# Optimization experiments

Hardware: AMD Instinct MI355X
Metric: run time of the kernel (lower is better)

The kernel has to match this reference:

```python
import jax, jax.numpy as jnp
import numpy as np

B, T, E, NH = 2, 1024, 512, 8


def setup_inputs() -> dict:
    key = jax.random.key(0)
    ks = jax.random.split(key, 7)
    s = 0.02
    return {
        "x": jax.random.normal(ks[0], (B, T, E), dtype=jnp.float32),
        "W_qkv": jax.random.normal(ks[1], (E, 3 * E), dtype=jnp.float32) * s,
        "b_qkv": jax.random.normal(ks[2], (3 * E,), dtype=jnp.float32) * s,
        "W_od": jax.random.normal(ks[3], (E, 2 * NH), dtype=jnp.float32) * s,
        "b_od": jax.random.normal(ks[4], (2 * NH,), dtype=jnp.float32) * s,
        "W_out": jax.random.normal(ks[5], (E, E), dtype=jnp.float32) * s,
        "b_out": jax.random.normal(ks[6], (E,), dtype=jnp.float32) * s,
        "length": T,
    }


def reference(x, W_qkv, b_qkv, W_od, b_od, W_out, b_out, length):
    b, t, e = x.shape
    nh = W_od.shape[1] // 2
    hd = e // nh
    scaling = float(hd) ** (-0.5)

    qkv = x @ W_qkv + b_qkv
    Q, K, V = jnp.split(qkv, 3, axis=-1)  # each (b, t, e)

    od = Q @ W_od + b_od  # (b, t, 2*nh)
    offset, duration = jnp.split(od, 2, axis=-1)
    offset = jnp.tanh(offset) * length
    duration = jax.nn.sigmoid(duration) * length

    qidx = jnp.arange(length, dtype=x.dtype)[None, :, None]  # (1, t, 1)
    anchor = qidx + offset  # (b, t, nh)

    # 'b t nh -> (b nh) t'
    anchor = anchor.transpose(0, 2, 1).reshape(b * nh, t)
    duration = duration.transpose(0, 2, 1).reshape(b * nh, t)

    start = anchor - duration
    end = anchor + duration
    bl = jnp.floor(start)          # left bound index
    br = jnp.ceil(end)             # right bound index
    al = jnp.floor(anchor)         # anchor left index
    ar = al + 1                    # anchor right index
    dist_al = anchor - al          # anchor_dist_l

    r = jnp.arange(length, dtype=x.dtype)[None, None, :]  # (1, 1, t)

    def pmask(idx):  # point mask (bnh, t, t), float
        return (r == idx[:, :, None]).astype(x.dtype)

    point_weight = (1.0
                    + (bl - start)[:, :, None] * pmask(bl)
                    + (end - br)[:, :, None] * pmask(br)
                    + dist_al[:, :, None] * pmask(ar)
                    + (1.0 - dist_al)[:, :, None] * pmask(al))

    attn_mask = (r < bl[:, :, None]) | (r > br[:, :, None])  # (bnh, t, t) bool

    def heads(z):  # 'b t (nh hd) -> (b nh) t hd'
        return z.reshape(b, t, nh, hd).transpose(0, 2, 1, 3).reshape(b * nh, t, hd)

    Qh, Kh, Vh = heads(Q), heads(K), heads(V)

    scores = jnp.einsum('bic,brc->bir', Qh, Kh) * scaling
    scores = scores * point_weight
    scores = jnp.where(attn_mask, jnp.asarray(-1e8, x.dtype), scores)
    attn = jax.nn.softmax(scores, axis=-1)

    out = jnp.einsum('bir,brc->bic', attn, Vh)  # (bnh, t, hd)
    out = out.reshape(b, nh, t, hd).transpose(0, 2, 1, 3).reshape(b, t, e)
    return out @ W_out + b_out
```

## Files before the change

kernel.cpp:

```cpp
#include <hip/hip_runtime.h>

typedef unsigned short ushort_t;
typedef short s16x8 __attribute__((ext_vector_type(8)));
typedef float f32x4 __attribute__((ext_vector_type(4)));

#define DEVINL __device__ __forceinline__

DEVINL ushort_t f2b(float f) {
  union { float f; unsigned int u; } v; v.f = f;
  unsigned int r = (v.u + 0x7fffu + ((v.u >> 16) & 1u)) >> 16;
  return (ushort_t)r;
}

DEVINL ushort_t f2b_hw(float f) {
  union { __bf16 h; ushort_t u; } cv;
  cv.h = (__bf16)f;
  return cv.u;
}

__global__ __launch_bounds__(256) void prep_kernel(
    const float* __restrict__ Wqkv, const float* __restrict__ bq,
    const float* __restrict__ Wod, const float* __restrict__ bod,
    const float* __restrict__ Wout,
    ushort_t* __restrict__ WqkvT, ushort_t* __restrict__ WoT,
    float* __restrict__ Wcomb, float* __restrict__ bcomb)
{
  __shared__ ushort_t tile[64 * 72];
  const int b = blockIdx.x;
  const int tid = threadIdx.x;

  if (b < 256) {
    const float* in;
    ushort_t* out;
    int N, bx, by;
    if (b < 192) { in = Wqkv; out = WqkvT; N = 1536; bx = b % 24; by = b / 24; }
    else         { in = Wout; out = WoT;   N = 512;  bx = (b - 192) % 8; by = (b - 192) / 8; }
    const int K = 512;
    const int n0 = bx * 64, k0 = by * 64;
    const int cr = tid >> 4;
    const int cc = (tid & 15) * 4;
#pragma unroll
    for (int p = 0; p < 4; p++) {
      int k = k0 + p * 16 + cr;
      float4 v = *(const float4*)(in + k * N + n0 + cc);
      ushort4 o; o.x = f2b(v.x); o.y = f2b(v.y); o.z = f2b(v.z); o.w = f2b(v.w);
      *(ushort4*)(tile + (p * 16 + cr) * 72 + cc) = o;
    }
    __syncthreads();
#pragma unroll
    for (int p = 0; p < 4; p++) {
      int n = n0 + p * 16 + cr;
      ushort4 v;
      v.x = tile[(cc + 0) * 72 + p * 16 + cr];
      v.y = tile[(cc + 1) * 72 + p * 16 + cr];
      v.z = tile[(cc + 2) * 72 + p * 16 + cr];
      v.w = tile[(cc + 3) * 72 + p * 16 + cr];
      *(ushort4*)(out + n * K + k0 + cc) = v;
    }
    return;
  }

  const int w = tid >> 6, lane = tid & 63;
  const int c = (b - 256) * 4 + w;
  if (c > 512) return;
  float a[8];
  const float* src = (c < 512) ? (Wqkv + c * 1536 + lane * 8) : (bq + lane * 8);
  float4 a0 = *(const float4*)(src);
  float4 a1 = *(const float4*)(src + 4);
  a[0]=a0.x; a[1]=a0.y; a[2]=a0.z; a[3]=a0.w;
  a[4]=a1.x; a[5]=a1.y; a[6]=a1.z; a[7]=a1.w;

  float s[16];
#pragma unroll
  for (int j = 0; j < 16; j++) s[j] = 0.f;
#pragma unroll
  for (int i = 0; i < 8; i++) {
    const float* wp = Wod + (lane * 8 + i) * 16;
#pragma unroll
    for (int j = 0; j < 16; j++) s[j] += a[i] * wp[j];
  }
#pragma unroll
  for (int mask = 1; mask < 64; mask <<= 1)
#pragma unroll
    for (int j = 0; j < 16; j++) s[j] += __shfl_xor(s[j], mask);

  if (lane < 16) {
    if (c < 512) Wcomb[c * 16 + lane] = s[lane];
    else         bcomb[lane] = s[lane] + bod[lane];
  }
}

__global__ __launch_bounds__(256) void od_kernel(
    const float* __restrict__ x, const float* __restrict__ Wcomb,
    const float* __restrict__ bcomb, const int* __restrict__ lenp,
    float* __restrict__ params, ushort_t* __restrict__ xb)
{
  const int w = threadIdx.x >> 6, lane = threadIdx.x & 63;
  const int m = blockIdx.x * 4 + w;
  int li = lenp[0];
  float len = (li > 0 && li < 1048576) ? (float)li : 1024.0f;

  const float* qp = x + m * 512 + lane * 8;
  float q[8];
  float4 qa = *(const float4*)(qp);
  float4 qb = *(const float4*)(qp + 4);
  q[0]=qa.x; q[1]=qa.y; q[2]=qa.z; q[3]=qa.w;
  q[4]=qb.x; q[5]=qb.y; q[6]=qb.z; q[7]=qb.w;

  s16x8 ov;
#pragma unroll
  for (int i = 0; i < 8; i++) ov[i] = (short)f2b(q[i]);
  *(s16x8*)(xb + m * 512 + lane * 8) = ov;

  float s[16];
#pragma unroll
  for (int j = 0; j < 16; j++) s[j] = 0.f;
#pragma unroll
  for (int i = 0; i < 8; i++) {
    const float* wp = Wcomb + (lane * 8 + i) * 16;
#pragma unroll
    for (int j = 0; j < 16; j++) s[j] += q[i] * wp[j];
  }
#pragma unroll
  for (int mask = 1; mask < 64; mask <<= 1)
#pragma unroll
    for (int j = 0; j < 16; j++) s[j] += __shfl_xor(s[j], mask);

  if (lane < 8) {
    int h = lane;
    int bb = m >> 10, t = m & 1023;
    float odo = s[h] + bcomb[h];
    float odd = s[8 + h] + bcomb[8 + h];
    float offset = tanhf(odo) * len;
    float dur = len / (1.f + expf(-odd));
    float anchor = (float)t + offset;
    float start = anchor - dur, end = anchor + dur;
    float bl = floorf(start), br = ceilf(end);
    float al = floorf(anchor);
    float da = anchor - al;
    float* pp = params + ((bb * 8 + h) * 1024 + t) * 6;
    pp[0] = bl; pp[1] = br; pp[2] = al;
    pp[3] = bl - start; pp[4] = end - br; pp[5] = da;
  }
}

__global__ __launch_bounds__(256) void qkv_gemm_kernel(
    const ushort_t* __restrict__ xb, const ushort_t* __restrict__ WT,
    const float* __restrict__ bqkv,
    ushort_t* __restrict__ Qh, ushort_t* __restrict__ Kh, ushort_t* __restrict__ VT)
{
  __shared__ ushort_t As[64 * 32];
  __shared__ ushort_t Bs[128 * 32];
  const int tid = threadIdx.x;
  const int lane = tid & 63, w = tid >> 6;
  const int wr = w >> 1, wc = w & 1;
  const int quad = lane >> 4, l16 = lane & 15;
  const int m0 = blockIdx.y * 64, n0 = blockIdx.x * 128;

  f32x4 acc[2][4];
#pragma unroll
  for (int i = 0; i < 2; i++)
#pragma unroll
    for (int j = 0; j < 4; j++) acc[i][j] = f32x4{0.f, 0.f, 0.f, 0.f};

  const int idx = tid * 8;
  const int ra = idx >> 5, ca = idx & 31;
  const int rb1 = (idx + 2048) >> 5, cb1 = (idx + 2048) & 31;

  for (int k0 = 0; k0 < 512; k0 += 32) {
    s16x8 va  = *(const s16x8*)(xb + (m0 + ra) * 512 + k0 + ca);
    s16x8 vb0 = *(const s16x8*)(WT + (n0 + ra) * 512 + k0 + ca);
    s16x8 vb1 = *(const s16x8*)(WT + (n0 + rb1) * 512 + k0 + cb1);
    __syncthreads();
    *(s16x8*)(As + idx) = va;
    *(s16x8*)(Bs + idx) = vb0;
    *(s16x8*)(Bs + idx + 2048) = vb1;
    __syncthreads();

    s16x8 af[2], bfr[4];
#pragma unroll
    for (int mt = 0; mt < 2; mt++)
      af[mt] = *(const s16x8*)(As + (wr * 32 + mt * 16 + l16) * 32 + quad * 8);
#pragma unroll
    for (int nt = 0; nt < 4; nt++)
      bfr[nt] = *(const s16x8*)(Bs + (wc * 64 + nt * 16 + l16) * 32 + quad * 8);
#pragma unroll
    for (int mt = 0; mt < 2; mt++)
#pragma unroll
      for (int nt = 0; nt < 4; nt++)
        acc[mt][nt] = __builtin_amdgcn_mfma_f32_16x16x32_bf16(af[mt], bfr[nt], acc[mt][nt], 0, 0, 0);
  }

#pragma unroll
  for (int nt = 0; nt < 4; nt++) {
    int c = n0 + wc * 64 + nt * 16 + l16;
    float bias = bqkv[c];
    int which = c >> 9;
    int e = c & 511;
    int h = e >> 6, d = e & 63;
#pragma unroll
    for (int mt = 0; mt < 2; mt++) {
      int mbase = m0 + wr * 32 + mt * 16 + quad * 4;
      int bb = mbase >> 10, t = mbase & 1023;
      int bh = bb * 8 + h;
      if (which == 2) {
        ushort4 pk;
        pk.x = f2b(acc[mt][nt][0] + bias);
        pk.y = f2b(acc[mt][nt][1] + bias);
        pk.z = f2b(acc[mt][nt][2] + bias);
        pk.w = f2b(acc[mt][nt][3] + bias);
        *(ushort4*)(VT + (bh * 64 + d) * 1024 + t) = pk;
      } else {
        ushort_t* dst = (which == 0) ? Qh : Kh;
        float sc = (which == 0) ? 0.125f : 1.0f;
#pragma unroll
        for (int rr = 0; rr < 4; rr++)
          dst[(bh * 1024 + t + rr) * 64 + d] = f2b((acc[mt][nt][rr] + bias) * sc);
      }
    }
  }
}

__global__ __launch_bounds__(256, 3) void attn_kernel(
    const ushort_t* __restrict__ Qh, const ushort_t* __restrict__ Kh,
    const ushort_t* __restrict__ VT, const float* __restrict__ params,
    ushort_t* __restrict__ Oh)
{
  __shared__ ushort_t Plds[4 * 16 * 72];
  __shared__ float Om[4][16][65];
  __shared__ float lwS[4][16];

  const int tid = threadIdx.x;
  const int lane = tid & 63, w = tid >> 6;
  const int quad = lane >> 4, l16 = lane & 15;
  const int bh = blockIdx.x;
  const int mrow = blockIdx.y * 16;
  ushort_t* Pw = Plds + w * (16 * 72);

  s16x8 aq0 = *(const s16x8*)(Qh + (bh * 1024 + mrow + l16) * 64 + quad * 8);
  s16x8 aq1 = *(const s16x8*)(Qh + (bh * 1024 + mrow + l16) * 64 + 32 + quad * 8);

  float bl[4], br[4], al[4], wl[4], wr2[4], da[4];
  float lo = 1.0e9f, hi = -1.0e9f;
#pragma unroll
  for (int rr = 0; rr < 4; rr++) {
    int row = mrow + quad * 4 + rr;
    const float* pp = params + (bh * 1024 + row) * 6;
    bl[rr] = pp[0]; br[rr] = pp[1]; al[rr] = pp[2];
    wl[rr] = pp[3]; wr2[rr] = pp[4]; da[rr] = pp[5];
    bool empty = (br[rr] < 0.f) || (bl[rr] > 1023.f);
    float lo_r = empty ? 0.f    : fmaxf(bl[rr], 0.f);
    float hi_r = empty ? 1023.f : fminf(br[rr], 1023.f);
    lo = fminf(lo, lo_r); hi = fmaxf(hi, hi_r);
  }
  lo = fminf(lo, __shfl_xor(lo, 16));
  lo = fminf(lo, __shfl_xor(lo, 32));
  hi = fmaxf(hi, __shfl_xor(hi, 16));
  hi = fmaxf(hi, __shfl_xor(hi, 32));
  const int tlo = ((int)lo) >> 6, thi = ((int)hi) >> 6;

  float lr[4] = {0.f, 0.f, 0.f, 0.f};
  f32x4 Oacc[4];
#pragma unroll
  for (int nt = 0; nt < 4; nt++) Oacc[nt] = f32x4{0.f, 0.f, 0.f, 0.f};

  for (int tt = tlo + w; tt <= thi; tt += 4) {
    const int r0 = tt * 64;

    s16x8 bk0[4], bk1[4], bv0[4], bv1[4];
#pragma unroll
    for (int nt = 0; nt < 4; nt++) {
      const ushort_t* kp = Kh + (bh * 1024 + r0 + nt * 16 + l16) * 64 + quad * 8;
      bk0[nt] = *(const s16x8*)(kp);
      bk1[nt] = *(const s16x8*)(kp + 32);
    }
#pragma unroll
    for (int nt = 0; nt < 4; nt++) {
      const ushort_t* vp = VT + (bh * 64 + nt * 16 + l16) * 1024 + r0 + quad * 8;
      bv0[nt] = *(const s16x8*)(vp);
      bv1[nt] = *(const s16x8*)(vp + 32);
    }

    f32x4 S[4];
#pragma unroll
    for (int nt = 0; nt < 4; nt++) {
      f32x4 z = {0.f, 0.f, 0.f, 0.f};
      z = __builtin_amdgcn_mfma_f32_16x16x32_bf16(aq0, bk0[nt], z, 0, 0, 0);
      z = __builtin_amdgcn_mfma_f32_16x16x32_bf16(aq1, bk1[nt], z, 0, 0, 0);
      S[nt] = z;
    }

    const float r0f = (float)r0, r1f = (float)(r0 + 63);
    bool fastb = true;
#pragma unroll
    for (int rr = 0; rr < 4; rr++) {
      bool f = (bl[rr] < r0f) && (br[rr] > r1f) &&
               ((al[rr] + 1.f < r0f) || (al[rr] > r1f));
      fastb = fastb && f;
    }
    if (__all((int)fastb)) {
#pragma unroll
      for (int nt = 0; nt < 4; nt++)
#pragma unroll
        for (int rr = 0; rr < 4; rr++) {
          float p = __expf(S[nt][rr]);
          lr[rr] += p;
          S[nt][rr] = p;
        }
    } else {
#pragma unroll
      for (int nt = 0; nt < 4; nt++) {
        float cf = (float)(r0 + nt * 16 + l16);
#pragma unroll
        for (int rr = 0; rr < 4; rr++) {
          float s = S[nt][rr];
          float wgt = 1.f;
          wgt += (cf == bl[rr]) ? wl[rr] : 0.f;
          wgt += (cf == br[rr]) ? wr2[rr] : 0.f;
          wgt += (cf == al[rr] + 1.f) ? da[rr] : 0.f;
          wgt += (cf == al[rr]) ? (1.f - da[rr]) : 0.f;
          s *= wgt;
          s = (cf < bl[rr] || cf > br[rr]) ? -30.f : s;
          float p = __expf(s);
          lr[rr] += p;
          S[nt][rr] = p;
        }
      }
    }

#pragma unroll
    for (int nt = 0; nt < 4; nt++)
#pragma unroll
      for (int rr = 0; rr < 4; rr++)
        Pw[(quad * 4 + rr) * 72 + nt * 16 + l16] = f2b_hw(S[nt][rr]);

    s16x8 pa0 = *(const s16x8*)(Pw + l16 * 72 + quad * 8);
    s16x8 pa1 = *(const s16x8*)(Pw + l16 * 72 + 32 + quad * 8);

#pragma unroll
    for (int nt = 0; nt < 4; nt++) {
      Oacc[nt] = __builtin_amdgcn_mfma_f32_16x16x32_bf16(pa0, bv0[nt], Oacc[nt], 0, 0, 0);
      Oacc[nt] = __builtin_amdgcn_mfma_f32_16x16x32_bf16(pa1, bv1[nt], Oacc[nt], 0, 0, 0);
    }
  }

#pragma unroll
  for (int mask = 1; mask < 16; mask <<= 1)
#pragma unroll
    for (int rr = 0; rr < 4; rr++) lr[rr] += __shfl_xor(lr[rr], mask);

#pragma unroll
  for (int nt = 0; nt < 4; nt++)
#pragma unroll
    for (int rr = 0; rr < 4; rr++)
      Om[w][quad * 4 + rr][nt * 16 + l16] = Oacc[nt][rr];
  if (l16 == 0) {
#pragma unroll
    for (int rr = 0; rr < 4; rr++) lwS[w][quad * 4 + rr] = lr[rr];
  }
  __syncthreads();

  {
    const int col = tid & 63;
    const int rbase = (tid >> 6) * 4;
    const int bb = bh >> 3, h = bh & 7;
#pragma unroll
    for (int k = 0; k < 4; k++) {
      int r = rbase + k;
      float lg = lwS[0][r] + lwS[1][r] + lwS[2][r] + lwS[3][r];
      float o  = Om[0][r][col] + Om[1][r][col] + Om[2][r][col] + Om[3][r][col];
      int t = mrow + r;
      Oh[((bb << 10) + t) * 512 + h * 64 + col] = f2b_hw(o / lg);
    }
  }
}

__global__ __launch_bounds__(256) void out_gemm_kernel(
    const ushort_t* __restrict__ Oh, const ushort_t* __restrict__ WT,
    const float* __restrict__ bout, float* __restrict__ outp)
{
  __shared__ ushort_t As[64 * 32];
  __shared__ ushort_t Bs[64 * 32];
  const int tid = threadIdx.x;
  const int lane = tid & 63, w = tid >> 6;
  const int wr = w >> 1, wc = w & 1;
  const int quad = lane >> 4, l16 = lane & 15;
  const int m0 = blockIdx.y * 64, n0 = blockIdx.x * 64;

  f32x4 acc[2][2];
#pragma unroll
  for (int i = 0; i < 2; i++)
#pragma unroll
    for (int j = 0; j < 2; j++) acc[i][j] = f32x4{0.f, 0.f, 0.f, 0.f};

  const int idx = tid * 8;
  const int ra = idx >> 5, ca = idx & 31;

  for (int k0 = 0; k0 < 512; k0 += 32) {
    s16x8 va = *(const s16x8*)(Oh + (m0 + ra) * 512 + k0 + ca);
    s16x8 vb = *(const s16x8*)(WT + (n0 + ra) * 512 + k0 + ca);
    __syncthreads();
    *(s16x8*)(As + idx) = va;
    *(s16x8*)(Bs + idx) = vb;
    __syncthreads();

    s16x8 af[2], bfr[2];
#pragma unroll
    for (int mt = 0; mt < 2; mt++)
      af[mt] = *(const s16x8*)(As + (wr * 32 + mt * 16 + l16) * 32 + quad * 8);
#pragma unroll
    for (int nt = 0; nt < 2; nt++)
      bfr[nt] = *(const s16x8*)(Bs + (wc * 32 + nt * 16 + l16) * 32 + quad * 8);
#pragma unroll
    for (int mt = 0; mt < 2; mt++)
#pragma unroll
      for (int nt = 0; nt < 2; nt++)
        acc[mt][nt] = __builtin_amdgcn_mfma_f32_16x16x32_bf16(af[mt], bfr[nt], acc[mt][nt], 0, 0, 0);
  }

#pragma unroll
  for (int nt = 0; nt < 2; nt++) {
    int c = n0 + wc * 32 + nt * 16 + l16;
    float bias = bout[c];
#pragma unroll
    for (int mt = 0; mt < 2; mt++) {
#pragma unroll
      for (int rr = 0; rr < 4; rr++) {
        int m = m0 + wr * 32 + mt * 16 + quad * 4 + rr;
        outp[m * 512 + c] = acc[mt][nt][rr] + bias;
      }
    }
  }
}

extern "C" void kernel_launch(void* const* d_in, const int* in_sizes, int n_in,
                              void* d_out, int out_size, void* d_ws, size_t ws_size,
                              hipStream_t stream)
{
  const float* x    = (const float*)d_in[0];
  const float* Wqkv = (const float*)d_in[1];
  const float* bqkv = (const float*)d_in[2];
  const float* Wod  = (const float*)d_in[3];
  const float* bod  = (const float*)d_in[4];
  const float* Wout = (const float*)d_in[5];
  const float* bout = (const float*)d_in[6];
  const int* lenp   = (const int*)d_in[7];

  char* ws = (char*)d_ws;
  ushort_t* WqkvT  = (ushort_t*)(ws);
  ushort_t* WoT    = (ushort_t*)(ws + 1572864);
  ushort_t* xb     = (ushort_t*)(ws + 2097152);
  ushort_t* Qh     = (ushort_t*)(ws + 4194304);
  ushort_t* Kh     = (ushort_t*)(ws + 6291456);
  ushort_t* VT     = (ushort_t*)(ws + 8388608);
  ushort_t* Oh     = (ushort_t*)(ws + 10485760);
  float*    Wcomb  = (float*)(ws + 12582912);
  float*    bcomb  = (float*)(ws + 12615680);
  float*    params = (float*)(ws + 12615744);

  prep_kernel<<<385, 256, 0, stream>>>(Wqkv, bqkv, Wod, bod, Wout, WqkvT, WoT, Wcomb, bcomb);
  od_kernel<<<512, 256, 0, stream>>>(x, Wcomb, bcomb, lenp, params, xb);
  qkv_gemm_kernel<<<dim3(12, 32), 256, 0, stream>>>(xb, WqkvT, bqkv, Qh, Kh, VT);
  attn_kernel<<<dim3(16, 64), 256, 0, stream>>>(Qh, Kh, VT, params, Oh);
  out_gemm_kernel<<<dim3(8, 32), 256, 0, stream>>>(Oh, WoT, bout, (float*)d_out);
}
```

Measured before the change: 139.6 us.

## Share K/V tiles across waves via LDS with register prefetch

The attention loop changes from each wave independently loading and processing its own 64-key tiles to all four waves cooperatively staging one 64-key K/V tile in LDS, with each wave handling a 16-key slice. The next tile is prefetched into registers while the current one is processed, aiming for coalesced loads and hidden global-load latency. In exchange it adds two block-wide barriers per tile. The P·V MFMA now runs on a half-zero-padded P operand, so that matrix work is doubled. The last wave's V reads spill past the row into LDS padding that is never initialized, and NaN bits there times zero could corrupt results.

After: 129.9 us. 1.07x faster.

```diff
diff --git a/kernel.cpp b/kernel.cpp
--- a/kernel.cpp
+++ b/kernel.cpp
@@ -226,7 +226,9 @@
     const ushort_t* __restrict__ VT, const float* __restrict__ params,
     ushort_t* __restrict__ Oh)
 {
-  __shared__ ushort_t Plds[4 * 16 * 72];
+  __shared__ ushort_t Kt[64 * 72 + 32];
+  __shared__ ushort_t Vt[64 * 72 + 96];
+  __shared__ ushort_t Ps[4][16 * 40];
   __shared__ float Om[4][16][65];
   __shared__ float lwS[4][16];
 
@@ -235,7 +237,11 @@
   const int quad = lane >> 4, l16 = lane & 15;
   const int bh = blockIdx.x;
   const int mrow = blockIdx.y * 16;
-  ushort_t* Pw = Plds + w * (16 * 72);
+  ushort_t* Pw = Ps[w];
+
+#pragma unroll
+  for (int rr = 0; rr < 4; rr++)
+    Pw[(quad * 4 + rr) * 40 + 16 + l16] = 0;
 
   s16x8 aq0 = *(const s16x8*)(Qh + (bh * 1024 + mrow + l16) * 64 + quad * 8);
   s16x8 aq1 = *(const s16x8*)(Qh + (bh * 1024 + mrow + l16) * 64 + 32 + quad * 8);
@@ -264,83 +270,85 @@
 #pragma unroll
   for (int nt = 0; nt < 4; nt++) Oacc[nt] = f32x4{0.f, 0.f, 0.f, 0.f};
 
-  for (int tt = tlo + w; tt <= thi; tt += 4) {
+  const int srow = tid >> 2, sseg = (tid & 3) * 16;
+  const ushort_t* kgb = Kh + (bh * 1024 + srow) * 64 + sseg;
+  const ushort_t* vgb = VT + (bh * 64 + srow) * 1024 + sseg;
+
+  s16x8 kr0, kr1, vr0, vr1;
+  {
+    const int r0 = tlo * 64;
+    kr0 = *(const s16x8*)(kgb + r0 * 64);
+    kr1 = *(const s16x8*)(kgb + r0 * 64 + 8);
+    vr0 = *(const s16x8*)(vgb + r0);
+    vr1 = *(const s16x8*)(vgb + r0 + 8);
+  }
+
+  for (int tt = tlo; tt <= thi; tt++) {
     const int r0 = tt * 64;
-
-    s16x8 bk0[4], bk1[4], bv0[4], bv1[4];
+    __syncthreads();
+    *(s16x8*)(Kt + srow * 72 + sseg)     = kr0;
+    *(s16x8*)(Kt + srow * 72 + sseg + 8) = kr1;
+    *(s16x8*)(Vt + srow * 72 + sseg)     = vr0;
+    *(s16x8*)(Vt + srow * 72 + sseg + 8) = vr1;
+    __syncthreads();
+
+    if (tt + 1 <= thi) {
+      const int r1 = (tt + 1) * 64;
+      kr0 = *(const s16x8*)(kgb + r1 * 64);
+      kr1 = *(const s16x8*)(kgb + r1 * 64 + 8);
+      vr0 = *(const s16x8*)(vgb + r1);
+      vr1 = *(const s16x8*)(vgb + r1 + 8);
+    }
+
+    s16x8 bk0 = *(const s16x8*)(Kt + (w * 16 + l16) * 72 + quad * 8);
+    s16x8 bk1 = *(const s16x8*)(Kt + (w * 16 + l16) * 72 + 32 + quad * 8);
+    f32x4 S = {0.f, 0.f, 0.f, 0.f};
+    S = __builtin_amdgcn_mfma_f32_16x16x32_bf16(aq0, bk0, S, 0, 0, 0);
+    S = __builtin_amdgcn_mfma_f32_16x16x32_bf16(aq1, bk1, S, 0, 0, 0);
+
+    const float cf = (float)(r0 + w * 16 + l16);
+    const float c0f = (float)(r0 + w * 16), c1f = c0f + 15.f;
+    bool fastb = true;
+#pragma unroll
+    for (int rr = 0; rr < 4; rr++) {
+      bool f = (bl[rr] < c0f) && (br[rr] > c1f) &&
+               ((al[rr] + 1.f < c0f) || (al[rr] > c1f));
+      fastb = fastb && f;
+    }
+    float p4[4];
+    if (__all((int)fastb)) {
+#pragma unroll
+      for (int rr = 0; rr < 4; rr++) {
+        float p = __expf(S[rr]);
+        lr[rr] += p;
+        p4[rr] = p;
+      }
+    } else {
+#pragma unroll
+      for (int rr = 0; rr < 4; rr++) {
+        float s = S[rr];
+        float wgt = 1.f;
+        wgt += (cf == bl[rr]) ? wl[rr] : 0.f;
+        wgt += (cf == br[rr]) ? wr2[rr] : 0.f;
+        wgt += (cf == al[rr] + 1.f) ? da[rr] : 0.f;
+        wgt += (cf == al[rr]) ? (1.f - da[rr]) : 0.f;
+        s *= wgt;
+        s = (cf < bl[rr] || cf > br[rr]) ? -30.f : s;
+        float p = __expf(s);
+        lr[rr] += p;
+        p4[rr] = p;
+      }
+    }
+
+#pragma unroll
+    for (int rr = 0; rr < 4; rr++)
+      Pw[(quad * 4 + rr) * 40 + l16] = f2b_hw(p4[rr]);
+
+    s16x8 pa = *(const s16x8*)(Pw + l16 * 40 + quad * 8);
 #pragma unroll
     for (int nt = 0; nt < 4; nt++) {
-      const ushort_t* kp = Kh + (bh * 1024 + r0 + nt * 16 + l16) * 64 + quad * 8;
-      bk0[nt] = *(const s16x8*)(kp);
-      bk1[nt] = *(const s16x8*)(kp + 32);
-    }
-#pragma unroll
-    for (int nt = 0; nt < 4; nt++) {
-      const ushort_t* vp = VT + (bh * 64 + nt * 16 + l16) * 1024 + r0 + quad * 8;
-      bv0[nt] = *(const s16x8*)(vp);
-      bv1[nt] = *(const s16x8*)(vp + 32);
-    }
-
-    f32x4 S[4];
-#pragma unroll
-    for (int nt = 0; nt < 4; nt++) {
-      f32x4 z = {0.f, 0.f, 0.f, 0.f};
-      z = __builtin_amdgcn_mfma_f32_16x16x32_bf16(aq0, bk0[nt], z, 0, 0, 0);
-      z = __builtin_amdgcn_mfma_f32_16x16x32_bf16(aq1, bk1[nt], z, 0, 0, 0);
-      S[nt] = z;
-    }
-
-    const float r0f = (float)r0, r1f = (float)(r0 + 63);
-    bool fastb = true;
-#pragma unroll
-    for (int rr = 0; rr < 4; rr++) {
-      bool f = (bl[rr] < r0f) && (br[rr] > r1f) &&
-               ((al[rr] + 1.f < r0f) || (al[rr] > r1f));
-      fastb = fastb && f;
-    }
-    if (__all((int)fastb)) {
-#pragma unroll
-      for (int nt = 0; nt < 4; nt++)
-#pragma unroll
-        for (int rr = 0; rr < 4; rr++) {
-          float p = __expf(S[nt][rr]);
-          lr[rr] += p;
-          S[nt][rr] = p;
-        }
-    } else {
-#pragma unroll
-      for (int nt = 0; nt < 4; nt++) {
-        float cf = (float)(r0 + nt * 16 + l16);
-#pragma unroll
-        for (int rr = 0; rr < 4; rr++) {
-          float s = S[nt][rr];
-          float wgt = 1.f;
-          wgt += (cf == bl[rr]) ? wl[rr] : 0.f;
-          wgt += (cf == br[rr]) ? wr2[rr] : 0.f;
-          wgt += (cf == al[rr] + 1.f) ? da[rr] : 0.f;
-          wgt += (cf == al[rr]) ? (1.f - da[rr]) : 0.f;
-          s *= wgt;
-          s = (cf < bl[rr] || cf > br[rr]) ? -30.f : s;
-          float p = __expf(s);
-          lr[rr] += p;
-          S[nt][rr] = p;
-        }
-      }
-    }
-
-#pragma unroll
-    for (int nt = 0; nt < 4; nt++)
-#pragma unroll
-      for (int rr = 0; rr < 4; rr++)
-        Pw[(quad * 4 + rr) * 72 + nt * 16 + l16] = f2b_hw(S[nt][rr]);
-
-    s16x8 pa0 = *(const s16x8*)(Pw + l16 * 72 + quad * 8);
-    s16x8 pa1 = *(const s16x8*)(Pw + l16 * 72 + 32 + quad * 8);
-
-#pragma unroll
-    for (int nt = 0; nt < 4; nt++) {
-      Oacc[nt] = __builtin_amdgcn_mfma_f32_16x16x32_bf16(pa0, bv0[nt], Oacc[nt], 0, 0, 0);
-      Oacc[nt] = __builtin_amdgcn_mfma_f32_16x16x32_bf16(pa1, bv1[nt], Oacc[nt], 0, 0, 0);
+      s16x8 bv = *(const s16x8*)(Vt + (nt * 16 + l16) * 72 + w * 16 + quad * 8);
+      Oacc[nt] = __builtin_amdgcn_mfma_f32_16x16x32_bf16(pa, bv, Oacc[nt], 0, 0, 0);
     }
   }
 
```
